# Optimization experiments

Measured on AMD Instinct MI355X. Metric: run time of the kernel, lower is better.

## Reference

```python
import jax, jax.numpy as jnp
import numpy as np

N = 100000   # num_entities
R = 8        # num_relations
B = 8        # num_bases = min(R, 30)
D = 128      # hidden_dim == embedding_dim
E = 800000   # num_edges


def rgcn_layer(x, edge_index, edge_type, basis, comp, root, bias):
    """PyG-style RGCNConv with basis decomposition and per-relation mean aggregation.

    Mean aggregation is linear, so we aggregate raw source features per
    (dst, relation) segment first, then apply the relation transform once
    per (node, relation) instead of per edge.
    """
    n, r = x.shape[0], comp.shape[0]
    W = jnp.einsum('rb,bio->rio', comp, basis)          # [R, D_in, D_out]
    src, dst = edge_index[0], edge_index[1]
    seg = dst * r + edge_type                            # segment key per edge
    agg = jax.ops.segment_sum(x[src], seg, num_segments=n * r)          # [N*R, D_in]
    cnt = jax.ops.segment_sum(jnp.ones((src.shape[0],), x.dtype), seg,
                              num_segments=n * r)                        # [N*R]
    agg = (agg / jnp.maximum(cnt, 1.0)[:, None]).reshape(n, r, -1)       # [N, R, D_in]
    return jnp.einsum('nri,rio->no', agg, W) + x @ root + bias


def setup_inputs() -> dict:
    key = jax.random.key(0)
    ks = jax.random.split(key, 12)
    s_in = 1.0 / np.sqrt(D)
    inp = {
        'edge_index': jax.random.randint(ks[0], (2, E), 0, N, dtype=jnp.int64 if jax.config.jax_enable_x64 else jnp.int32),
        'edge_type': jax.random.randint(ks[1], (E,), 0, R, dtype=jnp.int64 if jax.config.jax_enable_x64 else jnp.int32),
        'emb': jax.random.normal(ks[2], (N, D), jnp.float32) * s_in,
        'basis1': jax.random.normal(ks[3], (B, D, D), jnp.float32) * s_in,
        'comp1': jax.random.normal(ks[4], (R, B), jnp.float32) * (1.0 / np.sqrt(B)),
        'root1': jax.random.normal(ks[5], (D, D), jnp.float32) * s_in,
        'bias1': jnp.zeros((D,), jnp.float32),
        'basis2': jax.random.normal(ks[6], (B, D, D), jnp.float32) * s_in,
        'comp2': jax.random.normal(ks[7], (R, B), jnp.float32) * (1.0 / np.sqrt(B)),
        'root2': jax.random.normal(ks[8], (D, D), jnp.float32) * s_in,
        'bias2': jnp.zeros((D,), jnp.float32),
    }
    return inp


def reference(edge_index, edge_type, emb, basis1, comp1, root1, bias1,
              basis2, comp2, root2, bias2):
    # layer 1 + ReLU (dropout is identity at eval time)
    x = rgcn_layer(emb, edge_index, edge_type, basis1, comp1, root1, bias1)
    x = jax.nn.relu(x)
    # layer 2 (output layer, no activation)
    x = rgcn_layer(x, edge_index, edge_type, basis2, comp2, root2, bias2)
    return x
```

## Files before the change

kernel.cpp:

```cpp
#include <hip/hip_runtime.h>

#define NN 100000
#define RR 8
#define BB 8
#define DD 128
#define EE 800000
#define KT 1152
#define NBLK 782
#define NSEG2 (NBLK * 1024)
#define ASTR 40
#define AESTR 40
#define ECH 192

typedef __attribute__((ext_vector_type(8))) __bf16 bf16x8;
typedef __attribute__((ext_vector_type(4))) float f32x4;
typedef __attribute__((ext_vector_type(4))) unsigned int u32x4;

__device__ __forceinline__ unsigned short f2bf(float f) {
    unsigned u = __float_as_uint(f);
    u += 0x7fffu + ((u >> 16) & 1u);
    return (unsigned short)(u >> 16);
}
__device__ __forceinline__ float bf2f(unsigned short h) {
    return __uint_as_float(((unsigned)h) << 16);
}

__global__ __launch_bounds__(256) void k_cvt(const float* __restrict__ x,
                                             unsigned short* __restrict__ xh) {
    int i = blockIdx.x * 256 + threadIdx.x;
    f32x4 a = ((const f32x4*)x)[2 * i];
    f32x4 b = ((const f32x4*)x)[2 * i + 1];
    u32x4 o;
    o[0] = (unsigned)f2bf(a[0]) | ((unsigned)f2bf(a[1]) << 16);
    o[1] = (unsigned)f2bf(a[2]) | ((unsigned)f2bf(a[3]) << 16);
    o[2] = (unsigned)f2bf(b[0]) | ((unsigned)f2bf(b[1]) << 16);
    o[3] = (unsigned)f2bf(b[2]) | ((unsigned)f2bf(b[3]) << 16);
    ((u32x4*)xh)[i] = o;
}

__global__ __launch_bounds__(256) void k_cnt(const int* __restrict__ ei,
                                             const int* __restrict__ et,
                                             int* __restrict__ cnt) {
    int e = blockIdx.x * 256 + threadIdx.x;
    if (e < EE) {
        int d = ei[EE + e];
        atomicAdd(&cnt[(d >> 7) * 1024 + et[e] * 128 + (d & 127)], 1);
    }
}

__global__ __launch_bounds__(256) void k_scan_local(const int* __restrict__ cnt,
                                                    int* __restrict__ loc,
                                                    int* __restrict__ bsum) {
    __shared__ int tmp[256];
    int t = threadIdx.x, i = blockIdx.x * 256 + t;
    int v = cnt[i];
    tmp[t] = v; __syncthreads();
    int val = v;
#pragma unroll
    for (int d = 1; d < 256; d <<= 1) {
        int a = (t >= d) ? tmp[t - d] : 0;
        __syncthreads();
        val += a; tmp[t] = val;
        __syncthreads();
    }
    loc[i] = val - v;
    if (t == 255) bsum[blockIdx.x] = val;
}

__global__ void k_scan_bsum(const int* __restrict__ bsum, int* __restrict__ boff) {
    __shared__ int tmp[256];
    const int NB = NSEG2 / 256;
    const int CH = 13;
    int t = threadIdx.x;
    int base = t * CH, s = 0;
    for (int j = 0; j < CH; ++j) { int idx = base + j; if (idx < NB) s += bsum[idx]; }
    tmp[t] = s; __syncthreads();
    int val = s;
#pragma unroll
    for (int d = 1; d < 256; d <<= 1) {
        int a = (t >= d) ? tmp[t - d] : 0;
        __syncthreads();
        val += a; tmp[t] = val;
        __syncthreads();
    }
    int run = val - s;
    for (int j = 0; j < CH; ++j) { int idx = base + j; if (idx < NB) { boff[idx] = run; run += bsum[idx]; } }
}

__global__ __launch_bounds__(256) void k_scan_add(int* __restrict__ loc,
                                                  const int* __restrict__ boff) {
    int i = blockIdx.x * 256 + threadIdx.x;
    loc[i] += boff[i >> 8];
}

__global__ __launch_bounds__(256) void k_roff(const int* __restrict__ segoff,
                                              int* __restrict__ roff) {
    int idx = blockIdx.x * 256 + threadIdx.x;
    if (idx < NBLK * 8) roff[idx] = segoff[(idx >> 3) * 1024 + (idx & 7) * 128];
    if (idx == NBLK * 8) roff[idx] = EE;
}

__global__ __launch_bounds__(256) void k_scatter(const int* __restrict__ ei,
                                                 const int* __restrict__ et,
                                                 int* __restrict__ segoff,
                                                 int* __restrict__ spk) {
    int e = blockIdx.x * 256 + threadIdx.x;
    if (e < EE) {
        int d = ei[EE + e];
        int key = (d >> 7) * 1024 + et[e] * 128 + (d & 127);
        int pos = atomicAdd(&segoff[key], 1);
        spk[pos] = ei[e];
    }
}

__global__ __launch_bounds__(256) void k_prepB(const float* __restrict__ root,
                                               const float* __restrict__ comp,
                                               const float* __restrict__ basis,
                                               unsigned short* __restrict__ Bhi,
                                               unsigned short* __restrict__ Blo) {
    int idx = blockIdx.x * 256 + threadIdx.x;
    if (idx >= DD * KT) return;
    int o = idx / KT, k = idx - o * KT;
    float v;
    if (k < DD) {
        v = root[k * DD + o];
    } else {
        int r = (k - DD) >> 7, i = (k - DD) & 127;
        float s = 0.f;
#pragma unroll
        for (int b = 0; b < BB; ++b)
            s += comp[r * BB + b] * basis[((size_t)b * DD + i) * DD + o];
        v = s;
    }
    unsigned short hi = f2bf(v);
    Bhi[idx] = hi;
    Blo[idx] = f2bf(v - bf2f(hi));
}

template <bool WRITE_H1>
__global__ __launch_bounds__(256, 3) void k_gemm(
    const unsigned short* __restrict__ xh,
    const unsigned short* __restrict__ Bhi,
    const unsigned short* __restrict__ Blo,
    const float* __restrict__ bias,
    const int* __restrict__ spk,
    const int* __restrict__ roff,
    const int* __restrict__ segend,
    const int* __restrict__ cnt,
    unsigned short* __restrict__ h1h,
    float* __restrict__ outf)
{
    __shared__ unsigned short As[128 * ASTR];
    __shared__ unsigned short Bhs[128 * ASTR];
    __shared__ unsigned short Bls[128 * ASTR];
    __shared__ unsigned short Ae[ECH * AESTR];
    __shared__ int sbeg[1024];
    __shared__ unsigned short scnt[1024];
    __shared__ int reb[9];

    const int tid = threadIdx.x;
    const int b = blockIdx.x;
    const int M0 = b * 128;

    if (tid < 9) reb[tid] = roff[b * 8 + tid];
#pragma unroll
    for (int p = 0; p < 4; ++p) {
        int i = p * 256 + tid;
        int end = segend[b * 1024 + i];
        int c = cnt[b * 1024 + i];
        sbeg[i] = end - c;
        scnt[i] = (unsigned short)c;
    }

    const int wave = tid >> 6, lane = tid & 63;
    const int quad = lane >> 4, lm = lane & 15;
    const int erow = tid >> 1, half = tid & 1;

    float bv[8];
#pragma unroll
    for (int nt = 0; nt < 8; ++nt) bv[nt] = bias[nt * 16 + lm];

    f32x4 acc[2][8];
#pragma unroll
    for (int a = 0; a < 2; ++a)
#pragma unroll
        for (int n = 0; n < 8; ++n) acc[a][n] = (f32x4){0.f, 0.f, 0.f, 0.f};

    __syncthreads();

    for (int ks = 0; ks < KT / 32; ++ks) {
        const int k0 = ks * 32;

        if (ks < 4) {
            int nidx = M0 + erow; if (nidx > NN - 1) nidx = NN - 1;
            const u32x4* px = (const u32x4*)(xh + (size_t)nidx * DD + k0 + half * 16);
            u32x4 a0 = px[0], a1 = px[1];
            __syncthreads();
            unsigned short* pa = &As[erow * ASTR + half * 16];
            *(u32x4*)pa = a0;
            *(u32x4*)(pa + 8) = a1;
        } else {
            const int r = (ks - 4) >> 2;
            const int i0 = ((ks - 4) & 3) * 32;
            const int rb = reb[r], rend = reb[r + 1];
            const int si = r * 128 + erow;
            const int beg = sbeg[si];
            const int cs = scnt[si];
            const int send_ = beg + cs;

            float v[16];
#pragma unroll
            for (int j = 0; j < 16; ++j) v[j] = 0.f;

            if (rb >= rend) __syncthreads();
            for (int cb0 = rb; cb0 < rend; cb0 += ECH) {
                u32x4 a0 = {}, a1 = {}, a2 = {}, a3 = {};
                const int e = cb0 + tid;
                const bool have = (tid < ECH) && (e < rend);
                if (have) {
                    const int s = spk[e];
                    const u32x4* px = (const u32x4*)(xh + (size_t)s * DD + i0);
                    a0 = px[0]; a1 = px[1]; a2 = px[2]; a3 = px[3];
                }
                __syncthreads();
                if (have) {
                    u32x4* pe = (u32x4*)&Ae[tid * AESTR];
                    pe[0] = a0; pe[1] = a1; pe[2] = a2; pe[3] = a3;
                }
                __syncthreads();
                int lo = beg > cb0 ? beg : cb0;
                int hi2 = send_ < cb0 + ECH ? send_ : cb0 + ECH;
                for (int e2 = lo; e2 < hi2; ++e2) {
                    const unsigned* pe = (const unsigned*)&Ae[(e2 - cb0) * AESTR + half * 16];
#pragma unroll
                    for (int q = 0; q < 8; ++q) {
                        unsigned u = pe[q];
                        v[2 * q]     += __uint_as_float(u << 16);
                        v[2 * q + 1] += __uint_as_float(u & 0xFFFF0000u);
                    }
                }
            }
            const float inv = 1.0f / (float)(cs > 1 ? cs : 1);
            unsigned pk8[8];
#pragma unroll
            for (int j = 0; j < 8; ++j)
                pk8[j] = (unsigned)f2bf(v[2 * j] * inv) | ((unsigned)f2bf(v[2 * j + 1] * inv) << 16);
            unsigned short* pa = &As[erow * ASTR + half * 16];
            *(u32x4*)pa = (u32x4){pk8[0], pk8[1], pk8[2], pk8[3]};
            *(u32x4*)(pa + 8) = (u32x4){pk8[4], pk8[5], pk8[6], pk8[7]};
        }

#pragma unroll
        for (int p = 0; p < 2; ++p) {
            int c2 = p * 256 + tid;
            int o = c2 >> 2, q = c2 & 3;
            int goff = o * KT + k0 + q * 8;
            *(u32x4*)&Bhs[o * ASTR + q * 8] = *(const u32x4*)(Bhi + goff);
            *(u32x4*)&Bls[o * ASTR + q * 8] = *(const u32x4*)(Blo + goff);
        }
        __syncthreads();

        bf16x8 af0 = __builtin_bit_cast(bf16x8, *(const u32x4*)&As[(wave * 32 + lm) * ASTR + quad * 8]);
        bf16x8 af1 = __builtin_bit_cast(bf16x8, *(const u32x4*)&As[(wave * 32 + 16 + lm) * ASTR + quad * 8]);
#pragma unroll
        for (int nt = 0; nt < 8; ++nt) {
            bf16x8 bh = __builtin_bit_cast(bf16x8, *(const u32x4*)&Bhs[(nt * 16 + lm) * ASTR + quad * 8]);
            bf16x8 bl = __builtin_bit_cast(bf16x8, *(const u32x4*)&Bls[(nt * 16 + lm) * ASTR + quad * 8]);
            acc[0][nt] = __builtin_amdgcn_mfma_f32_16x16x32_bf16(af0, bh, acc[0][nt], 0, 0, 0);
            acc[0][nt] = __builtin_amdgcn_mfma_f32_16x16x32_bf16(af0, bl, acc[0][nt], 0, 0, 0);
            acc[1][nt] = __builtin_amdgcn_mfma_f32_16x16x32_bf16(af1, bh, acc[1][nt], 0, 0, 0);
            acc[1][nt] = __builtin_amdgcn_mfma_f32_16x16x32_bf16(af1, bl, acc[1][nt], 0, 0, 0);
        }
    }

#pragma unroll
    for (int mt = 0; mt < 2; ++mt) {
#pragma unroll
        for (int nt = 0; nt < 8; ++nt) {
#pragma unroll
            for (int rg = 0; rg < 4; ++rg) {
                int row = M0 + wave * 32 + mt * 16 + quad * 4 + rg;
                if (row < NN) {
                    int col = nt * 16 + lm;
                    float v = acc[mt][nt][rg] + bv[nt];
                    if (WRITE_H1) h1h[(size_t)row * DD + col] = f2bf(fmaxf(v, 0.f));
                    else          outf[(size_t)row * DD + col] = v;
                }
            }
        }
    }
}


extern "C" void kernel_launch(void* const* d_in, const int* in_sizes, int n_in,
                              void* d_out, int out_size, void* d_ws, size_t ws_size,
                              hipStream_t stream) {
    const int*   ei     = (const int*)d_in[0];
    const int*   et     = (const int*)d_in[1];
    const float* emb    = (const float*)d_in[2];
    const float* basis1 = (const float*)d_in[3];
    const float* comp1  = (const float*)d_in[4];
    const float* root1  = (const float*)d_in[5];
    const float* bias1  = (const float*)d_in[6];
    const float* basis2 = (const float*)d_in[7];
    const float* comp2  = (const float*)d_in[8];
    const float* root2  = (const float*)d_in[9];
    const float* bias2  = (const float*)d_in[10];
    float* out = (float*)d_out;
    (void)in_sizes; (void)n_in; (void)out_size; (void)ws_size;

    char* ws = (char*)d_ws;
    int*            cnt    = (int*)(ws + 0);
    int*            segoff = (int*)(ws + 3203072);
    int*            spk    = (int*)(ws + 6406144);
    int*            bsum   = (int*)(ws + 9606144);
    int*            boff   = (int*)(ws + 9618656);
    int*            roffp  = (int*)(ws + 9631168);
    unsigned short* Bhi1   = (unsigned short*)(ws + 9656320);
    unsigned short* Blo1   = (unsigned short*)(ws + 9951232);
    unsigned short* Bhi2   = (unsigned short*)(ws + 10246144);
    unsigned short* Blo2   = (unsigned short*)(ws + 10541056);
    unsigned short* embh   = (unsigned short*)(ws + 10835968);
    unsigned short* h1h    = (unsigned short*)(ws + 36435968);

    hipMemsetAsync(cnt, 0, (size_t)NSEG2 * 4, stream);

    k_cvt       <<<NN * DD / (256 * 8), 256, 0, stream>>>(emb, embh);
    k_cnt       <<<(EE + 255) / 256, 256, 0, stream>>>(ei, et, cnt);
    k_scan_local<<<NSEG2 / 256, 256, 0, stream>>>(cnt, segoff, bsum);
    k_scan_bsum <<<1, 256, 0, stream>>>(bsum, boff);
    k_scan_add  <<<NSEG2 / 256, 256, 0, stream>>>(segoff, boff);
    k_roff      <<<(NBLK * 8 + 256) / 256, 256, 0, stream>>>(segoff, roffp);
    k_scatter   <<<(EE + 255) / 256, 256, 0, stream>>>(ei, et, segoff, spk);

    k_prepB<<<(DD * KT + 255) / 256, 256, 0, stream>>>(root1, comp1, basis1, Bhi1, Blo1);
    k_prepB<<<(DD * KT + 255) / 256, 256, 0, stream>>>(root2, comp2, basis2, Bhi2, Blo2);

    k_gemm<true> <<<NBLK, 256, 0, stream>>>(embh, Bhi1, Blo1, bias1, spk, roffp, segoff, cnt, h1h, nullptr);
    k_gemm<false><<<NBLK, 256, 0, stream>>>(h1h,  Bhi2, Blo2, bias2, spk, roffp, segoff, cnt, nullptr, out);
}
```

Before: 565.9 us.

## Prefetch next relation's first edge chunk into registers across k-steps

Restructures the k-loop into a root phase and a per-relation phase. The first ECH edges of each relation's full 128-wide source rows are gathered into a 16-vector register stage, issued one relation ahead and overlapped with the MFMA work. This removes the exposed gather latency for the common single-chunk case. In exchange it adds 64 VGPRs of staging per thread, which may lower occupancy or cause spills.

After: 750.4 us. +32.6%, slower.

```diff
diff --git a/kernel.cpp b/kernel.cpp
--- a/kernel.cpp
+++ b/kernel.cpp
@@ -186,70 +186,9 @@
 #pragma unroll
         for (int n = 0; n < 8; ++n) acc[a][n] = (f32x4){0.f, 0.f, 0.f, 0.f};
 
-    __syncthreads();
-
-    for (int ks = 0; ks < KT / 32; ++ks) {
-        const int k0 = ks * 32;
-
-        if (ks < 4) {
-            int nidx = M0 + erow; if (nidx > NN - 1) nidx = NN - 1;
-            const u32x4* px = (const u32x4*)(xh + (size_t)nidx * DD + k0 + half * 16);
-            u32x4 a0 = px[0], a1 = px[1];
-            __syncthreads();
-            unsigned short* pa = &As[erow * ASTR + half * 16];
-            *(u32x4*)pa = a0;
-            *(u32x4*)(pa + 8) = a1;
-        } else {
-            const int r = (ks - 4) >> 2;
-            const int i0 = ((ks - 4) & 3) * 32;
-            const int rb = reb[r], rend = reb[r + 1];
-            const int si = r * 128 + erow;
-            const int beg = sbeg[si];
-            const int cs = scnt[si];
-            const int send_ = beg + cs;
-
-            float v[16];
-#pragma unroll
-            for (int j = 0; j < 16; ++j) v[j] = 0.f;
-
-            if (rb >= rend) __syncthreads();
-            for (int cb0 = rb; cb0 < rend; cb0 += ECH) {
-                u32x4 a0 = {}, a1 = {}, a2 = {}, a3 = {};
-                const int e = cb0 + tid;
-                const bool have = (tid < ECH) && (e < rend);
-                if (have) {
-                    const int s = spk[e];
-                    const u32x4* px = (const u32x4*)(xh + (size_t)s * DD + i0);
-                    a0 = px[0]; a1 = px[1]; a2 = px[2]; a3 = px[3];
-                }
-                __syncthreads();
-                if (have) {
-                    u32x4* pe = (u32x4*)&Ae[tid * AESTR];
-                    pe[0] = a0; pe[1] = a1; pe[2] = a2; pe[3] = a3;
-                }
-                __syncthreads();
-                int lo = beg > cb0 ? beg : cb0;
-                int hi2 = send_ < cb0 + ECH ? send_ : cb0 + ECH;
-                for (int e2 = lo; e2 < hi2; ++e2) {
-                    const unsigned* pe = (const unsigned*)&Ae[(e2 - cb0) * AESTR + half * 16];
-#pragma unroll
-                    for (int q = 0; q < 8; ++q) {
-                        unsigned u = pe[q];
-                        v[2 * q]     += __uint_as_float(u << 16);
-                        v[2 * q + 1] += __uint_as_float(u & 0xFFFF0000u);
-                    }
-                }
-            }
-            const float inv = 1.0f / (float)(cs > 1 ? cs : 1);
-            unsigned pk8[8];
-#pragma unroll
-            for (int j = 0; j < 8; ++j)
-                pk8[j] = (unsigned)f2bf(v[2 * j] * inv) | ((unsigned)f2bf(v[2 * j + 1] * inv) << 16);
-            unsigned short* pa = &As[erow * ASTR + half * 16];
-            *(u32x4*)pa = (u32x4){pk8[0], pk8[1], pk8[2], pk8[3]};
-            *(u32x4*)(pa + 8) = (u32x4){pk8[4], pk8[5], pk8[6], pk8[7]};
-        }
-
+    u32x4 stg[16];
+
+    auto kstep_tail = [&](int k0) {
 #pragma unroll
         for (int p = 0; p < 2; ++p) {
             int c2 = p * 256 + tid;
@@ -270,6 +209,121 @@
             acc[0][nt] = __builtin_amdgcn_mfma_f32_16x16x32_bf16(af0, bl, acc[0][nt], 0, 0, 0);
             acc[1][nt] = __builtin_amdgcn_mfma_f32_16x16x32_bf16(af1, bh, acc[1][nt], 0, 0, 0);
             acc[1][nt] = __builtin_amdgcn_mfma_f32_16x16x32_bf16(af1, bl, acc[1][nt], 0, 0, 0);
+        }
+    };
+
+    __syncthreads();
+
+#pragma unroll
+    for (int ks = 0; ks < 4; ++ks) {
+        const int k0 = ks * 32;
+        int nidx = M0 + erow; if (nidx > NN - 1) nidx = NN - 1;
+        const u32x4* px = (const u32x4*)(xh + (size_t)nidx * DD + k0 + half * 16);
+        u32x4 a0 = px[0], a1 = px[1];
+        __syncthreads();
+        unsigned short* pa = &As[erow * ASTR + half * 16];
+        *(u32x4*)pa = a0;
+        *(u32x4*)(pa + 8) = a1;
+        if (ks == 0) {
+            const int rb0 = reb[0], re0 = reb[1];
+            const int e = rb0 + tid;
+            if (tid < ECH && e < re0) {
+                const int sp = spk[e];
+                const u32x4* ps = (const u32x4*)(xh + (size_t)sp * DD);
+#pragma unroll
+                for (int j = 0; j < 16; ++j) stg[j] = ps[j];
+            }
+        }
+        kstep_tail(k0);
+    }
+
+    for (int r = 0; r < RR; ++r) {
+        const int rb = reb[r], rend = reb[r + 1];
+        const int si = r * 128 + erow;
+        const int beg = sbeg[si];
+        const int cs = scnt[si];
+        const int send_ = beg + cs;
+
+#pragma unroll
+        for (int s = 0; s < 4; ++s) {
+            const int k0 = DD + r * 128 + s * 32;
+            const int i0 = s * 32;
+
+            float v[16];
+#pragma unroll
+            for (int j = 0; j < 16; ++j) v[j] = 0.f;
+
+            __syncthreads();
+            if (tid < ECH) {
+                u32x4* pe = (u32x4*)&Ae[tid * AESTR];
+                pe[0] = stg[4 * s + 0];
+                pe[1] = stg[4 * s + 1];
+                pe[2] = stg[4 * s + 2];
+                pe[3] = stg[4 * s + 3];
+            }
+            if (s == 3 && r + 1 < RR) {
+                const int nrb = reb[r + 1], nre = reb[r + 2];
+                const int e = nrb + tid;
+                if (tid < ECH && e < nre) {
+                    const int sp = spk[e];
+                    const u32x4* ps = (const u32x4*)(xh + (size_t)sp * DD);
+#pragma unroll
+                    for (int j = 0; j < 16; ++j) stg[j] = ps[j];
+                }
+            }
+            __syncthreads();
+            {
+                int lo = beg > rb ? beg : rb;
+                int hi2 = send_ < rb + ECH ? send_ : rb + ECH;
+                for (int e2 = lo; e2 < hi2; ++e2) {
+                    const unsigned* pe = (const unsigned*)&Ae[(e2 - rb) * AESTR + half * 16];
+#pragma unroll
+                    for (int q = 0; q < 8; ++q) {
+                        unsigned u = pe[q];
+                        v[2 * q]     += __uint_as_float(u << 16);
+                        v[2 * q + 1] += __uint_as_float(u & 0xFFFF0000u);
+                    }
+                }
+            }
+
+            for (int cb0 = rb + ECH; cb0 < rend; cb0 += ECH) {
+                u32x4 a0 = {}, a1 = {}, a2 = {}, a3 = {};
+                const int e = cb0 + tid;
+                const bool have = (tid < ECH) && (e < rend);
+                if (have) {
+                    const int sp = spk[e];
+                    const u32x4* px = (const u32x4*)(xh + (size_t)sp * DD + i0);
+                    a0 = px[0]; a1 = px[1]; a2 = px[2]; a3 = px[3];
+                }
+                __syncthreads();
+                if (have) {
+                    u32x4* pe = (u32x4*)&Ae[tid * AESTR];
+                    pe[0] = a0; pe[1] = a1; pe[2] = a2; pe[3] = a3;
+                }
+                __syncthreads();
+                int lo = beg > cb0 ? beg : cb0;
+                int hi2 = send_ < cb0 + ECH ? send_ : cb0 + ECH;
+                for (int e2 = lo; e2 < hi2; ++e2) {
+                    const unsigned* pe = (const unsigned*)&Ae[(e2 - cb0) * AESTR + half * 16];
+#pragma unroll
+                    for (int q = 0; q < 8; ++q) {
+                        unsigned u = pe[q];
+                        v[2 * q]     += __uint_as_float(u << 16);
+                        v[2 * q + 1] += __uint_as_float(u & 0xFFFF0000u);
+                    }
+                }
+            }
+
+            const float inv = 1.0f / (float)(cs > 1 ? cs : 1);
+            unsigned pk8[8];
+#pragma unroll
+            for (int j = 0; j < 8; ++j)
+                pk8[j] = (unsigned)f2bf(v[2 * j] * inv) | ((unsigned)f2bf(v[2 * j + 1] * inv) << 16);
+            unsigned short* pa = &As[erow * ASTR + half * 16];
+            *(u32x4*)pa = (u32x4){pk8[0], pk8[1], pk8[2], pk8[3]};
+            *(u32x4*)(pa + 8) = (u32x4){pk8[4], pk8[5], pk8[6], pk8[7]};
+
+            kstep_tail(k0);
         }
     }
 
```

## Gather neighbor rows directly per thread instead of staging chunks through LDS

Applied to the files above, without the earlier changes.

The per-relation neighbor aggregation no longer loads 192-edge chunks of source rows into a shared staging buffer with two barriers per chunk. Each thread pair now walks its own segment's edges, reading a full 64-element half-row per edge from global memory, and accumulates all 128 columns once per relation. The four 32-wide K slices are then written to the A tile from registers. This removes LDS staging traffic and barriers, and each row is gathered once per relation rather than once per K slice. In exchange, register pressure grows (64 float accumulators per thread) and load balance across threads depends on segment sizes.

Result: slower. 690.8 us (+22.1%).

```diff
diff --git a/kernel.cpp b/kernel.cpp
--- a/kernel.cpp
+++ b/kernel.cpp
@@ -9,8 +9,6 @@
 #define NBLK 782
 #define NSEG2 (NBLK * 1024)
 #define ASTR 40
-#define AESTR 40
-#define ECH 192
 
 typedef __attribute__((ext_vector_type(8))) __bf16 bf16x8;
 typedef __attribute__((ext_vector_type(4))) float f32x4;
@@ -153,7 +151,6 @@
     __shared__ unsigned short As[128 * ASTR];
     __shared__ unsigned short Bhs[128 * ASTR];
     __shared__ unsigned short Bls[128 * ASTR];
-    __shared__ unsigned short Ae[ECH * AESTR];
     __shared__ int sbeg[1024];
     __shared__ unsigned short scnt[1024];
     __shared__ int reb[9];
@@ -186,70 +183,7 @@
 #pragma unroll
         for (int n = 0; n < 8; ++n) acc[a][n] = (f32x4){0.f, 0.f, 0.f, 0.f};
 
-    __syncthreads();
-
-    for (int ks = 0; ks < KT / 32; ++ks) {
-        const int k0 = ks * 32;
-
-        if (ks < 4) {
-            int nidx = M0 + erow; if (nidx > NN - 1) nidx = NN - 1;
-            const u32x4* px = (const u32x4*)(xh + (size_t)nidx * DD + k0 + half * 16);
-            u32x4 a0 = px[0], a1 = px[1];
-            __syncthreads();
-            unsigned short* pa = &As[erow * ASTR + half * 16];
-            *(u32x4*)pa = a0;
-            *(u32x4*)(pa + 8) = a1;
-        } else {
-            const int r = (ks - 4) >> 2;
-            const int i0 = ((ks - 4) & 3) * 32;
-            const int rb = reb[r], rend = reb[r + 1];
-            const int si = r * 128 + erow;
-            const int beg = sbeg[si];
-            const int cs = scnt[si];
-            const int send_ = beg + cs;
-
-            float v[16];
-#pragma unroll
-            for (int j = 0; j < 16; ++j) v[j] = 0.f;
-
-            if (rb >= rend) __syncthreads();
-            for (int cb0 = rb; cb0 < rend; cb0 += ECH) {
-                u32x4 a0 = {}, a1 = {}, a2 = {}, a3 = {};
-                const int e = cb0 + tid;
-                const bool have = (tid < ECH) && (e < rend);
-                if (have) {
-                    const int s = spk[e];
-                    const u32x4* px = (const u32x4*)(xh + (size_t)s * DD + i0);
-                    a0 = px[0]; a1 = px[1]; a2 = px[2]; a3 = px[3];
-                }
-                __syncthreads();
-                if (have) {
-                    u32x4* pe = (u32x4*)&Ae[tid * AESTR];
-                    pe[0] = a0; pe[1] = a1; pe[2] = a2; pe[3] = a3;
-                }
-                __syncthreads();
-                int lo = beg > cb0 ? beg : cb0;
-                int hi2 = send_ < cb0 + ECH ? send_ : cb0 + ECH;
-                for (int e2 = lo; e2 < hi2; ++e2) {
-                    const unsigned* pe = (const unsigned*)&Ae[(e2 - cb0) * AESTR + half * 16];
-#pragma unroll
-                    for (int q = 0; q < 8; ++q) {
-                        unsigned u = pe[q];
-                        v[2 * q]     += __uint_as_float(u << 16);
-                        v[2 * q + 1] += __uint_as_float(u & 0xFFFF0000u);
-                    }
-                }
-            }
-            const float inv = 1.0f / (float)(cs > 1 ? cs : 1);
-            unsigned pk8[8];
-#pragma unroll
-            for (int j = 0; j < 8; ++j)
-                pk8[j] = (unsigned)f2bf(v[2 * j] * inv) | ((unsigned)f2bf(v[2 * j + 1] * inv) << 16);
-            unsigned short* pa = &As[erow * ASTR + half * 16];
-            *(u32x4*)pa = (u32x4){pk8[0], pk8[1], pk8[2], pk8[3]};
-            *(u32x4*)(pa + 8) = (u32x4){pk8[4], pk8[5], pk8[6], pk8[7]};
-        }
-
+    auto kstep_tail = [&](int k0) {
 #pragma unroll
         for (int p = 0; p < 2; ++p) {
             int c2 = p * 256 + tid;
@@ -270,6 +204,71 @@
             acc[0][nt] = __builtin_amdgcn_mfma_f32_16x16x32_bf16(af0, bl, acc[0][nt], 0, 0, 0);
             acc[1][nt] = __builtin_amdgcn_mfma_f32_16x16x32_bf16(af1, bh, acc[1][nt], 0, 0, 0);
             acc[1][nt] = __builtin_amdgcn_mfma_f32_16x16x32_bf16(af1, bl, acc[1][nt], 0, 0, 0);
+        }
+    };
+
+    __syncthreads();
+
+#pragma unroll
+    for (int ks = 0; ks < 4; ++ks) {
+        const int k0 = ks * 32;
+        int nidx = M0 + erow; if (nidx > NN - 1) nidx = NN - 1;
+        const u32x4* px = (const u32x4*)(xh + (size_t)nidx * DD + k0 + half * 16);
+        u32x4 a0 = px[0], a1 = px[1];
+        __syncthreads();
+        unsigned short* pa = &As[erow * ASTR + half * 16];
+        *(u32x4*)pa = a0;
+        *(u32x4*)(pa + 8) = a1;
+        kstep_tail(k0);
+    }
+
+    for (int r = 0; r < RR; ++r) {
+        const int si = r * 128 + erow;
+        const int beg = sbeg[si];
+        const int cs = scnt[si];
+        const int send_ = beg + cs;
+
+        float v[32];
+        float v2[32];
+#pragma unroll
+        for (int j = 0; j < 32; ++j) { v[j] = 0.f; v2[j] = 0.f; }
+        for (int e2 = beg; e2 < send_; ++e2) {
+            const int sp = spk[e2];
+            const u32x4* ps = (const u32x4*)(xh + (size_t)sp * DD + half * 64);
+            u32x4 c0 = ps[0], c1 = ps[1], c2 = ps[2], c3 = ps[3];
+            u32x4 c4 = ps[4], c5 = ps[5], c6 = ps[6], c7 = ps[7];
+            const u32x4 cc[8] = {c0, c1, c2, c3, c4, c5, c6, c7};
+#pragma unroll
+            for (int q = 0; q < 8; ++q) {
+#pragma unroll
+                for (int w = 0; w < 4; ++w) {
+                    unsigned u = cc[q][w];
+                    v[q * 4 + w]  += __uint_as_float(u << 16);
+                    v2[q * 4 + w] += __uint_as_float(u & 0xFFFF0000u);
+                }
+            }
+        }
+        const float inv = 1.0f / (float)(cs > 1 ? cs : 1);
+#pragma unroll
+        for (int j = 0; j < 32; ++j) { v[j] *= inv; v2[j] *= inv; }
+
+#pragma unroll
+        for (int s = 0; s < 4; ++s) {
+            const int k0 = DD + r * 128 + s * 32;
+            __syncthreads();
+            if (half == (s >> 1)) {
+                const int j0 = (s & 1) * 16;
+                unsigned pk[16];
+#pragma unroll
+                for (int i = 0; i < 16; ++i)
+                    pk[i] = (unsigned)f2bf(v[j0 + i]) | ((unsigned)f2bf(v2[j0 + i]) << 16);
+                unsigned short* pa = &As[erow * ASTR];
+                *(u32x4*)(pa + 0)  = (u32x4){pk[0],  pk[1],  pk[2],  pk[3]};
+                *(u32x4*)(pa + 8)  = (u32x4){pk[4],  pk[5],  pk[6],  pk[7]};
+                *(u32x4*)(pa + 16) = (u32x4){pk[8],  pk[9],  pk[10], pk[11]};
+                *(u32x4*)(pa + 24) = (u32x4){pk[12], pk[13], pk[14], pk[15]};
+            }
+            kstep_tail(k0);
         }
     }
 
```
